# Kernel optimization log

Hardware: AMD Instinct MI355X
Metric: run time of the kernel (lower is better)

The kernel has to match this reference:

```python
import jax, jax.numpy as jnp
import numpy as np

H = 4  # num_heads

def _ln(x, g, b):
    m = x.mean(-1, keepdims=True)
    v = ((x - m) ** 2).mean(-1, keepdims=True)
    return (x - m) * jax.lax.rsqrt(v + 1e-5) * g + b

def _mlp(x, w1, b1, w2, b2):
    return jax.nn.relu(x @ w1 + b1) @ w2 + b2

def _lin_att(q, k, v):
    # q,k,v: [BB, L, H, hd] ; linear (kernelized) attention, no softmax
    L = q.shape[1]
    qn = q / jnp.maximum(jnp.linalg.norm(q, axis=-1, keepdims=True), 1e-12)
    kn = k / jnp.maximum(jnp.linalg.norm(k, axis=-1, keepdims=True), 1e-12)
    kvs = jnp.einsum('blhm,blhd->bhmd', kn, v)
    num = jnp.einsum('bnhm,bhmd->bnhd', qn, kvs) + L * v
    den = jnp.einsum('bnhm,bhm->bnh', qn, kn.sum(axis=1))[..., None] + L
    return num / den

def _fast_attn(x4, w_qkv, w_op, b_op):
    # x4: [B,T,N,D]; spatial attention over N, temporal attention over T, concat, project
    B, T, N, D = x4.shape
    hd = D // H
    q, k, v = jnp.split(x4 @ w_qkv, 3, axis=-1)
    sh = lambda t: t.reshape(B * T, N, H, hd)
    out_s = _lin_att(sh(q), sh(k), sh(v)).reshape(B, T, N, D)
    th = lambda t: jnp.swapaxes(t, 1, 2).reshape(B * N, T, H, hd)
    out_t = jnp.swapaxes(_lin_att(th(q), th(k), th(v)).reshape(B, N, T, D), 1, 2)
    return jnp.concatenate([out_s, out_t], axis=-1) @ w_op + b_op

def _forward(x, W_in, b_in, adp, W_tp, b_tp, qkv_w, op_w, op_b, pw_w, pw_b,
             fc_w1, fc_b1, fc_w2, fc_b2, ln1_g, ln1_b, ln2_g, ln2_b,
             ep_w, ep_b, enc_w1, enc_b1, enc_w2, enc_b2, out_w, out_b):
    Nn, T, _ = x.shape
    xt = jnp.swapaxes(x, 0, 1)[None]                 # [1,T,N,in]
    h = xt @ W_in + b_in                             # input_proj -> [1,T,N,24]
    h = jnp.concatenate([h, adp[None]], axis=-1)     # + adaptive emb -> [1,T,N,104]
    h = h @ W_tp + b_tp                              # temporal_proj: 1x1 conv == pointwise linear
    graph = jnp.einsum('tnd,tmd->tnm', adp, adp)     # [T,N,N]
    graph = jax.nn.softmax(jax.nn.relu(graph), axis=-1)  # AvgPool(1,1) is identity
    # GraphPropagate (order=2, eval/no-dropout): [h, graph @ h]
    z1 = jnp.einsum('tni,btid->btnd', graph, h)
    att0 = _fast_attn(h, qkv_w[0], op_w[0], op_b[0])
    att1 = _fast_attn(z1, qkv_w[1], op_w[1], op_b[1])
    # scale = [1, 0.01]; note torch's in-place aliasing makes ln1 input = 2*x_glo
    g = h + att0 * (h @ pw_w[0] + pw_b[0]) + 0.01 * att1 * (att0 @ pw_w[1] + pw_b[1])
    h1 = _ln(2.0 * g, ln1_g, ln1_b)
    h2 = _ln(h1 + _mlp(h1, fc_w1, fc_b1, fc_w2, fc_b2), ln2_g, ln2_b)
    y = jnp.swapaxes(h2, 1, 2).reshape(1, Nn, T * h2.shape[-1]) @ ep_w + ep_b  # encoder_proj
    for i in range(enc_w1.shape[0]):                 # 3 residual MLP blocks
        y = y + _mlp(y, enc_w1[i], enc_b1[i], enc_w2[i], enc_b2[i])
    out = y @ out_w + out_b                          # [1,N,365]
    return out.reshape(Nn, T, 1)

def setup_inputs() -> dict:
    key = jax.random.key(0)
    ks = jax.random.split(key, 24)
    f = lambda i, shape, s=0.05: jax.random.normal(ks[i], shape, dtype=jnp.float32) * s
    D, T, N, IN = 104, 365, 400, 3
    return {
        'x': jax.random.normal(ks[0], (N, T, IN), dtype=jnp.float32),
        'W_in': f(1, (IN, 24)), 'b_in': f(2, (24,)),
        'adp': f(3, (T, N, 80)),
        'W_tp': f(4, (D, D)), 'b_tp': f(5, (D,)),
        'qkv_w': f(6, (2, D, 3 * D)),
        'op_w': f(7, (2, 2 * D, D)), 'op_b': f(8, (2, D)),
        'pw_w': f(9, (2, D, D)), 'pw_b': f(10, (2, D)),
        'fc_w1': f(11, (D, 2 * D)), 'fc_b1': f(12, (2 * D,)),
        'fc_w2': f(13, (2 * D, D)), 'fc_b2': f(14, (D,)),
        'ln1_g': jnp.ones((D,), jnp.float32), 'ln1_b': jnp.zeros((D,), jnp.float32),
        'ln2_g': jnp.ones((D,), jnp.float32), 'ln2_b': jnp.zeros((D,), jnp.float32),
        'ep_w': f(15, (T * D, D), 0.01), 'ep_b': f(16, (D,)),
        'enc_w1': f(17, (3, D, 2 * D)), 'enc_b1': f(18, (3, 2 * D)),
        'enc_w2': f(19, (3, 2 * D, D)), 'enc_b2': f(20, (3, D)),
        'out_w': f(21, (D, T)), 'out_b': f(22, (T,)),
    }

def reference(x, W_in, b_in, adp, W_tp, b_tp, qkv_w, op_w, op_b, pw_w, pw_b,
              fc_w1, fc_b1, fc_w2, fc_b2, ln1_g, ln1_b, ln2_g, ln2_b,
              ep_w, ep_b, enc_w1, enc_b1, enc_w2, enc_b2, out_w, out_b):
    return _forward(x, W_in, b_in, adp, W_tp, b_tp, qkv_w, op_w, op_b, pw_w, pw_b,
                    fc_w1, fc_b1, fc_w2, fc_b2, ln1_g, ln1_b, ln2_g, ln2_b,
                    ep_w, ep_b, enc_w1, enc_b1, enc_w2, enc_b2, out_w, out_b)
```

## Files before the change

### kernel.cpp

```cpp
#include <hip/hip_runtime.h>
#include <hip/hip_bf16.h>
#include <cstddef>

#define TT   365
#define NN   400
#define TN   (TT*NN)
#define HD   26
#define NH   4

#define CEILDIV(a,b) (((a)+(b)-1)/(b))

typedef __hip_bfloat16 bf16;
typedef short short8v __attribute__((ext_vector_type(8)));
typedef float float4v __attribute__((ext_vector_type(4)));
typedef float float16v __attribute__((ext_vector_type(16)));
__device__ __forceinline__ float b2f(bf16 v){ return __bfloat162float(v); }
__device__ __forceinline__ bf16  f2b(float v){ return __float2bfloat16(v); }

static constexpr size_t NB0 = (size_t)TN*104;
static constexpr size_t NB1 = (size_t)TN*104;
static constexpr size_t NB2 = (size_t)TN*312;
static constexpr size_t NB3 = (size_t)TN*104;
static constexpr size_t NBF = NB0+NB1+NB2+NB3;
static constexpr size_t NTILE   = (size_t)108*32;
static constexpr size_t NKVSB_S = (size_t)TT*NTILE;
static constexpr size_t NKVSB_T = (size_t)NN*NTILE;
static constexpr size_t NY      = (size_t)NN*104;
static constexpr size_t NW_TP   = 104*128;
static constexpr size_t NW_QKV  = 312*128;
static constexpr size_t NW_OP   = 104*224;
static constexpr size_t NW_PW   = 104*128;
static constexpr size_t NW_FC1  = 208*128;
static constexpr size_t NW_FC2  = 104*224;
static constexpr size_t NW_EPT  = (size_t)104*37960;
static constexpr size_t NWT     = NW_TP + 2*NW_QKV + 2*NW_OP + 2*NW_PW + NW_FC1 + NW_FC2 + NW_EPT;
static constexpr size_t WS_NEEDED = NBF*2 + (NKVSB_S+NKVSB_T)*2 + NY*4 + NWT*2;
static constexpr size_t NADP_ROWS = (size_t)TN + 64;
static constexpr size_t NADP = NADP_ROWS*96;
static constexpr size_t NHT  = ((size_t)TT*104 + 8)*448;
static_assert(NADP + NHT <= NB2, "z1 scratch must fit in B2");

__global__ void __launch_bounds__(256) prep_w(
    const float* __restrict__ W, bf16* __restrict__ Wt, int K, int Nc, int KP)
{
    int idx = blockIdx.x*256 + threadIdx.x;
    if (idx >= Nc*KP) return;
    int n = idx / KP, k = idx - n*KP;
    Wt[idx] = (k < K) ? f2b(W[(size_t)k*Nc + n]) : f2b(0.f);
}

__global__ void __launch_bounds__(256) prep_wT(
    const float* __restrict__ W, bf16* __restrict__ Wt)
{
    __shared__ float T[64][105];
    int k0 = blockIdx.x * 64;
    int tid = threadIdx.x;
    for (int idx = tid; idx < 64*104; idx += 256) {
        int r = idx / 104, c = idx - r*104;
        int k = k0 + r;
        T[r][c] = (k < 37960) ? W[(size_t)k*104 + c] : 0.f;
    }
    __syncthreads();
    for (int idx = tid; idx < 104*32; idx += 256) {
        int n = idx >> 5, kp = idx & 31;
        int k = kp*2;
        if (k0 + k + 1 < 37960 || k0 + k < 37960) {
            if (k0 + k < 37960) {
                bf16 lo = f2b(T[k][n]);
                bf16 hi = f2b(T[k+1][n]);
                uint v = ((uint)(*(ushort*)&hi) << 16) | (*(ushort*)&lo);
                if (k0 + k + 1 < 37960) *(uint*)(Wt + (size_t)n*37960 + k0 + k) = v;
                else Wt[(size_t)n*37960 + k0 + k] = lo;
            }
        }
    }
}

__global__ void __launch_bounds__(256) prep_adp(
    const float* __restrict__ adp, bf16* __restrict__ out)
{
    size_t i = (size_t)blockIdx.x*256 + threadIdx.x;
    if (i >= NADP) return;
    size_t row = i / 96; int e = (int)(i - row*96);
    float v = (row < TN && e < 80) ? adp[row*80 + e] : 0.f;
    out[i] = f2b(v);
}

__global__ void __launch_bounds__(256) ht_kernel(
    const bf16* __restrict__ h, bf16* __restrict__ hT)
{
    __shared__ bf16 As[64*106];
    int t = blockIdx.y, n0 = blockIdx.x*64;
    int tid = threadIdx.x;
    for (int idx = tid; idx < 64*52; idx += 256) {
        int r = idx / 52, k = idx - r*52;
        int n = n0 + r;
        uint v = 0;
        if (n < NN) v = *(const uint*)(h + ((size_t)t*NN + n)*104 + k*2);
        *(uint*)(&As[r*106 + k*2]) = v;
    }
    __syncthreads();
    for (int idx = tid; idx < 104*32; idx += 256) {
        int d = idx >> 5, np = idx & 31;
        int n = np*2;
        ushort lo = *(ushort*)&As[n*106 + d];
        ushort hi = *(ushort*)&As[(n+1)*106 + d];
        uint v = ((uint)hi << 16) | lo;
        *(uint*)(hT + ((size_t)t*104 + d)*448 + n0 + n) = v;
    }
}

__global__ void __launch_bounds__(128) hcat_kernel(
    const float* __restrict__ x, const float* __restrict__ W_in,
    const float* __restrict__ b_in, const float* __restrict__ adp,
    bf16* __restrict__ hcat)
{
    int bid = blockIdx.x;
    int t = bid / NN, n = bid - t*NN;
    int tid = threadIdx.x;
    if (tid < 24) {
        float s = b_in[tid];
        size_t xb = ((size_t)n*TT + t)*3;
        #pragma unroll
        for (int i = 0; i < 3; ++i) s += x[xb + i] * W_in[i*24 + tid];
        hcat[(size_t)bid*104 + tid] = f2b(s);
    } else if (tid < 104) {
        hcat[(size_t)bid*104 + tid] = f2b(adp[(size_t)bid*80 + (tid - 24)]);
    }
}

template<int KP>
__global__ void __launch_bounds__(256) gemm_mf(
    const bf16* __restrict__ A, int lda, int K,
    const bf16* __restrict__ Wt, const float* __restrict__ bias,
    bf16* __restrict__ C, int M, int Nc, int relu)
{
    constexpr int STR = KP + 8;
    constexpr int KPQ = KP/8;
    __shared__ bf16 As[64*STR];
    __shared__ bf16 Ws[64*STR];
    int m0 = blockIdx.x * 64;
    int c0 = blockIdx.y * 64;
    int tid = threadIdx.x;
    const int KQ = K/8;
    uint4 z4 = {0u,0u,0u,0u};
    for (int idx = tid; idx < 64*KPQ; idx += 256) {
        int r = idx / KPQ, q = idx - r*KPQ;
        int m = m0 + r;
        uint4 v = z4;
        if (m < M && q < KQ) v = *(const uint4*)(A + (size_t)m*lda + q*8);
        *(uint4*)(&As[r*STR + q*8]) = v;
    }
    for (int idx = tid; idx < 64*KPQ; idx += 256) {
        int r = idx / KPQ, q = idx - r*KPQ;
        int n = c0 + r;
        uint4 v = z4;
        if (n < Nc) v = *(const uint4*)(Wt + (size_t)n*KP + q*8);
        *(uint4*)(&Ws[r*STR + q*8]) = v;
    }
    __syncthreads();

    int lane = tid & 63, w = tid >> 6;
    int n16 = lane & 15, quad = lane >> 4;
    constexpr int KS = KP/32;
    short8v af[KS];
    #pragma unroll
    for (int s = 0; s < KS; ++s)
        af[s] = *(const short8v*)(&As[(16*w + n16)*STR + s*32 + quad*8]);
    float4v acc[4];
    #pragma unroll
    for (int ct = 0; ct < 4; ++ct) { float4v z = {0.f,0.f,0.f,0.f}; acc[ct] = z; }
    #pragma unroll
    for (int ct = 0; ct < 4; ++ct) {
        #pragma unroll
        for (int s = 0; s < KS; ++s) {
            short8v bfr = *(const short8v*)(&Ws[(ct*16 + n16)*STR + s*32 + quad*8]);
            acc[ct] = __builtin_amdgcn_mfma_f32_16x16x32_bf16(af[s], bfr, acc[ct], 0, 0, 0);
        }
    }
    #pragma unroll
    for (int ct = 0; ct < 4; ++ct) {
        int c = c0 + ct*16 + n16;
        if (c < Nc) {
            float b = bias ? bias[c] : 0.f;
            #pragma unroll
            for (int reg = 0; reg < 4; ++reg) {
                int m = m0 + 16*w + quad*4 + reg;
                if (m < M) {
                    float v = acc[ct][reg] + b;
                    if (relu) v = fmaxf(v, 0.f);
                    C[(size_t)m*Nc + c] = f2b(v);
                }
            }
        }
    }
}

__global__ void __launch_bounds__(256) gate_ln1(
    bf16* __restrict__ h, const bf16* __restrict__ att0, const bf16* __restrict__ att1,
    const bf16* __restrict__ w0t, const bf16* __restrict__ w1t, const float* __restrict__ pwb,
    const float* __restrict__ gamma, const float* __restrict__ beta)
{
    constexpr int STR = 136;
    __shared__ bf16 A0s[64*STR];
    __shared__ bf16 A1s[64*STR];
    __shared__ bf16 Ws[112*STR];
    __shared__ float prm[416];
    int m0 = blockIdx.x * 64;
    int tid = threadIdx.x;
    int lane = tid & 63, w = tid >> 6, n16 = lane & 15, quad = lane >> 4;
    uint4 z4 = {0u,0u,0u,0u};

    for (int idx = tid; idx < 64*16; idx += 256) {
        int r = idx >> 4, q = idx & 15;
        int m = m0 + r;
        uint4 v0 = z4, v1 = z4;
        if (m < TN && q < 13) {
            v0 = *(const uint4*)(h    + (size_t)m*104 + q*8);
            v1 = *(const uint4*)(att0 + (size_t)m*104 + q*8);
        }
        *(uint4*)(&A0s[r*STR + q*8]) = v0;
        *(uint4*)(&A1s[r*STR + q*8]) = v1;
    }
    for (int idx = tid; idx < 112*16; idx += 256) {
        int c = idx >> 4, q = idx & 15;
        uint4 v = z4;
        if (c < 104) v = *(const uint4*)(w0t + (size_t)c*128 + q*8);
        *(uint4*)(&Ws[c*STR + q*8]) = v;
    }
    for (int i = tid; i < 416; i += 256)
        prm[i] = (i < 208) ? pwb[i] : (i < 312 ? gamma[i-208] : beta[i-312]);
    __syncthreads();

    short8v a0f[4], a1f[4];
    #pragma unroll
    for (int s = 0; s < 4; ++s) {
        a0f[s] = *(const short8v*)(&A0s[(16*w + n16)*STR + s*32 + quad*8]);
        a1f[s] = *(const short8v*)(&A1s[(16*w + n16)*STR + s*32 + quad*8]);
    }
    float4v acc0[7], acc1[7];
    #pragma unroll
    for (int ct = 0; ct < 7; ++ct) { float4v z = {0.f,0.f,0.f,0.f}; acc0[ct] = z; acc1[ct] = z; }
    #pragma unroll
    for (int ct = 0; ct < 7; ++ct)
        #pragma unroll
        for (int s = 0; s < 4; ++s) {
            short8v bfr = *(const short8v*)(&Ws[(ct*16 + n16)*STR + s*32 + quad*8]);
            acc0[ct] = __builtin_amdgcn_mfma_f32_16x16x32_bf16(a0f[s], bfr, acc0[ct], 0, 0, 0);
        }
    __syncthreads();
    for (int idx = tid; idx < 112*16; idx += 256) {
        int c = idx >> 4, q = idx & 15;
        uint4 v = z4;
        if (c < 104) v = *(const uint4*)(w1t + (size_t)c*128 + q*8);
        *(uint4*)(&Ws[c*STR + q*8]) = v;
    }
    __syncthreads();
    #pragma unroll
    for (int ct = 0; ct < 7; ++ct)
        #pragma unroll
        for (int s = 0; s < 4; ++s) {
            short8v bfr = *(const short8v*)(&Ws[(ct*16 + n16)*STR + s*32 + quad*8]);
            acc1[ct] = __builtin_amdgcn_mfma_f32_16x16x32_bf16(a1f[s], bfr, acc1[ct], 0, 0, 0);
        }

    float sum[4] = {0.f,0.f,0.f,0.f};
    #pragma unroll
    for (int ct = 0; ct < 7; ++ct) {
        int c = ct*16 + n16;
        bool colok = c < 104;
        float b0 = colok ? prm[c] : 0.f;
        float b1 = colok ? prm[104 + c] : 0.f;
        #pragma unroll
        for (int reg = 0; reg < 4; ++reg) {
            int r = 16*w + quad*4 + reg;
            int m = m0 + r;
            float xv = 0.f;
            if (colok && m < TN) {
                float p0 = acc0[ct][reg] + b0;
                float p1 = acc1[ct][reg] + b1;
                float hv = b2f(A0s[r*STR + c]);
                float a0 = b2f(A1s[r*STR + c]);
                float a1 = b2f(att1[(size_t)m*104 + c]);
                xv = 2.f*(hv + a0*p0 + 0.01f*a1*p1);
            }
            acc0[ct][reg] = xv;
            sum[reg] += xv;
        }
    }
    #pragma unroll
    for (int reg = 0; reg < 4; ++reg) {
        float v = sum[reg];
        v += __shfl_xor(v,1,64); v += __shfl_xor(v,2,64);
        v += __shfl_xor(v,4,64); v += __shfl_xor(v,8,64);
        sum[reg] = v * (1.f/104.f);
    }
    float var[4] = {0.f,0.f,0.f,0.f};
    #pragma unroll
    for (int ct = 0; ct < 7; ++ct) {
        bool colok = (ct*16 + n16) < 104;
        #pragma unroll
        for (int reg = 0; reg < 4; ++reg) {
            if (colok) {
                float d = acc0[ct][reg] - sum[reg];
                acc0[ct][reg] = d;
                var[reg] += d*d;
            }
        }
    }
    #pragma unroll
    for (int reg = 0; reg < 4; ++reg) {
        float v = var[reg];
        v += __shfl_xor(v,1,64); v += __shfl_xor(v,2,64);
        v += __shfl_xor(v,4,64); v += __shfl_xor(v,8,64);
        var[reg] = rsqrtf(v * (1.f/104.f) + 1e-5f);
    }
    #pragma unroll
    for (int ct = 0; ct < 7; ++ct) {
        int c = ct*16 + n16;
        if (c < 104) {
            float g = prm[208 + c], be = prm[312 + c];
            #pragma unroll
            for (int reg = 0; reg < 4; ++reg) {
                int m = m0 + 16*w + quad*4 + reg;
                if (m < TN)
                    h[(size_t)m*104 + c] = f2b(acc0[ct][reg]*var[reg]*g + be);
            }
        }
    }
}

__global__ void __launch_bounds__(256) fc2_ln2(
    const bf16* __restrict__ hidden, const bf16* __restrict__ w2t, const float* __restrict__ b2,
    const bf16* __restrict__ h1, const float* __restrict__ gamma, const float* __restrict__ beta,
    bf16* __restrict__ h2)
{
    constexpr int STRA = 232;
    constexpr int STRW = 136;
    __shared__ bf16 As[64*STRA];
    __shared__ bf16 Ws[112*STRW];
    __shared__ float prm[312];
    int m0 = blockIdx.x * 64;
    int tid = threadIdx.x;
    int lane = tid & 63, w = tid >> 6, n16 = lane & 15, quad = lane >> 4;
    uint4 z4 = {0u,0u,0u,0u};

    for (int idx = tid; idx < 64*28; idx += 256) {
        int r = idx / 28, q = idx - r*28;
        int m = m0 + r;
        uint4 v = z4;
        if (m < TN && q < 26) v = *(const uint4*)(hidden + (size_t)m*208 + q*8);
        *(uint4*)(&As[r*STRA + q*8]) = v;
    }
    for (int idx = tid; idx < 112*16; idx += 256) {
        int c = idx >> 4, q = idx & 15;
        uint4 v = z4;
        if (c < 104) v = *(const uint4*)(w2t + (size_t)c*224 + q*8);
        *(uint4*)(&Ws[c*STRW + q*8]) = v;
    }
    for (int i = tid; i < 312; i += 256)
        prm[i] = (i < 104) ? b2[i] : (i < 208 ? gamma[i-104] : beta[i-208]);
    __syncthreads();

    short8v af[7];
    #pragma unroll
    for (int s = 0; s < 7; ++s)
        af[s] = *(const short8v*)(&As[(16*w + n16)*STRA + s*32 + quad*8]);
    float4v acc[7];
    #pragma unroll
    for (int ct = 0; ct < 7; ++ct) { float4v z = {0.f,0.f,0.f,0.f}; acc[ct] = z; }
    #pragma unroll
    for (int ct = 0; ct < 7; ++ct)
        #pragma unroll
        for (int s = 0; s < 4; ++s) {
            short8v bfr = *(const short8v*)(&Ws[(ct*16 + n16)*STRW + s*32 + quad*8]);
            acc[ct] = __builtin_amdgcn_mfma_f32_16x16x32_bf16(af[s], bfr, acc[ct], 0, 0, 0);
        }
    __syncthreads();
    for (int idx = tid; idx < 112*16; idx += 256) {
        int c = idx >> 4, q = idx & 15;
        uint4 v = z4;
        if (c < 104 && q < 12) v = *(const uint4*)(w2t + (size_t)c*224 + 128 + q*8);
        *(uint4*)(&Ws[c*STRW + q*8]) = v;
    }
    __syncthreads();
    #pragma unroll
    for (int ct = 0; ct < 7; ++ct)
        #pragma unroll
        for (int s = 4; s < 7; ++s) {
            short8v bfr = *(const short8v*)(&Ws[(ct*16 + n16)*STRW + (s-4)*32 + quad*8]);
            acc[ct] = __builtin_amdgcn_mfma_f32_16x16x32_bf16(af[s], bfr, acc[ct], 0, 0, 0);
        }

    float sum[4] = {0.f,0.f,0.f,0.f};
    #pragma unroll
    for (int ct = 0; ct < 7; ++ct) {
        int c = ct*16 + n16;
        bool colok = c < 104;
        float bb = colok ? prm[c] : 0.f;
        #pragma unroll
        for (int reg = 0; reg < 4; ++reg) {
            int m = m0 + 16*w + quad*4 + reg;
            float xv = 0.f;
            if (colok && m < TN)
                xv = b2f(h1[(size_t)m*104 + c]) + acc[ct][reg] + bb;
            acc[ct][reg] = xv;
            sum[reg] += xv;
        }
    }
    #pragma unroll
    for (int reg = 0; reg < 4; ++reg) {
        float v = sum[reg];
        v += __shfl_xor(v,1,64); v += __shfl_xor(v,2,64);
        v += __shfl_xor(v,4,64); v += __shfl_xor(v,8,64);
        sum[reg] = v * (1.f/104.f);
    }
    float var[4] = {0.f,0.f,0.f,0.f};
    #pragma unroll
    for (int ct = 0; ct < 7; ++ct) {
        bool colok = (ct*16 + n16) < 104;
        #pragma unroll
        for (int reg = 0; reg < 4; ++reg) {
            if (colok) {
                float d = acc[ct][reg] - sum[reg];
                acc[ct][reg] = d;
                var[reg] += d*d;
            }
        }
    }
    #pragma unroll
    for (int reg = 0; reg < 4; ++reg) {
        float v = var[reg];
        v += __shfl_xor(v,1,64); v += __shfl_xor(v,2,64);
        v += __shfl_xor(v,4,64); v += __shfl_xor(v,8,64);
        var[reg] = rsqrtf(v * (1.f/104.f) + 1e-5f);
    }
    #pragma unroll
    for (int ct = 0; ct < 7; ++ct) {
        int c = ct*16 + n16;
        if (c < 104) {
            float g = prm[104 + c], be = prm[208 + c];
            #pragma unroll
            for (int reg = 0; reg < 4; ++reg) {
                int m = m0 + 16*w + quad*4 + reg;
                if (m < TN)
                    h2[(size_t)m*104 + c] = f2b(acc[ct][reg]*var[reg]*g + be);
            }
        }
    }
}

__global__ void __launch_bounds__(256) ep_mf(
    const bf16* __restrict__ h2, const bf16* __restrict__ wt, float* __restrict__ y)
{
    constexpr int STR = 136;
    __shared__ bf16 As[64*STR];
    __shared__ bf16 Ws[64*STR];
    int m0 = blockIdx.x * 64;
    int c0 = blockIdx.y * 64;
    int t0 = blockIdx.z * 8;
    int t1 = min(TT, t0 + 8);
    int tid = threadIdx.x;
    int lane = tid & 63, w = tid >> 6, n16 = lane & 15, quad = lane >> 4;
    uint4 z4 = {0u,0u,0u,0u};

    float4v acc[4];
    #pragma unroll
    for (int ct = 0; ct < 4; ++ct) { float4v z = {0.f,0.f,0.f,0.f}; acc[ct] = z; }

    for (int t = t0; t < t1; ++t) {
        for (int idx = tid; idx < 64*16; idx += 256) {
            int r = idx >> 4, q = idx & 15;
            int m = m0 + r;
            uint4 va = z4;
            if (m < NN && q < 13) va = *(const uint4*)(h2 + ((size_t)t*NN + m)*104 + q*8);
            *(uint4*)(&As[r*STR + q*8]) = va;
            int c = c0 + r;
            uint4 vw = z4;
            if (c < 104 && q < 13) vw = *(const uint4*)(wt + (size_t)c*37960 + t*104 + q*8);
            *(uint4*)(&Ws[r*STR + q*8]) = vw;
        }
        __syncthreads();
        short8v af[4];
        #pragma unroll
        for (int s = 0; s < 4; ++s)
            af[s] = *(const short8v*)(&As[(16*w + n16)*STR + s*32 + quad*8]);
        #pragma unroll
        for (int ct = 0; ct < 4; ++ct) {
            #pragma unroll
            for (int s = 0; s < 4; ++s) {
                short8v bfr = *(const short8v*)(&Ws[(ct*16 + n16)*STR + s*32 + quad*8]);
                acc[ct] = __builtin_amdgcn_mfma_f32_16x16x32_bf16(af[s], bfr, acc[ct], 0, 0, 0);
            }
        }
        __syncthreads();
    }
    #pragma unroll
    for (int ct = 0; ct < 4; ++ct) {
        int c = c0 + ct*16 + n16;
        if (c < 104) {
            #pragma unroll
            for (int reg = 0; reg < 4; ++reg) {
                int m = m0 + 16*w + quad*4 + reg;
                if (m < NN) atomicAdd(&y[(size_t)m*104 + c], acc[ct][reg]);
            }
        }
    }
}

__global__ void __launch_bounds__(256) z1_mf(
    const bf16* __restrict__ adp_bf, const bf16* __restrict__ hT, bf16* __restrict__ z1)
{
    constexpr int SA = 104;
    constexpr int SP = 72;
    __shared__ bf16 As[64*SA];
    __shared__ bf16 Bt[64*SA];
    __shared__ bf16 Ht[112*SP];
    __shared__ bf16 P[64*SP];
    int t = blockIdx.y;
    int r0 = blockIdx.x * 64;
    int tid = threadIdx.x;
    int lane = tid & 63, w = tid >> 6, n16 = lane & 15, quad = lane >> 4;

    {
        const uint4* src = (const uint4*)(adp_bf + ((size_t)t*NN + r0)*96);
        for (int idx = tid; idx < 768; idx += 256) {
            int r = idx / 12, q = idx - r*12;
            *(uint4*)(&As[r*SA + q*8]) = src[idx];
        }
    }
    __syncthreads();
    short8v af[3];
    #pragma unroll
    for (int s = 0; s < 3; ++s)
        af[s] = *(const short8v*)(&As[(16*w + n16)*SA + s*32 + quad*8]);

    float4v onum[7];
    #pragma unroll
    for (int dt = 0; dt < 7; ++dt) { float4v z = {0.f,0.f,0.f,0.f}; onum[dt] = z; }
    float rs[4] = {0.f,0.f,0.f,0.f};

    for (int c0 = 0; c0 < NN; c0 += 64) {
        {
            const uint4* srcB = (const uint4*)(adp_bf + ((size_t)t*NN + c0)*96);
            for (int idx = tid; idx < 768; idx += 256) {
                int r = idx / 12, q = idx - r*12;
                *(uint4*)(&Bt[r*SA + q*8]) = srcB[idx];
            }
        }
        {
            const bf16* hb = hT + (size_t)t*104*448 + c0;
            for (int idx = tid; idx < 896; idx += 256) {
                int d = idx >> 3, q = idx & 7;
                *(uint4*)(&Ht[d*SP + q*8]) = *(const uint4*)(hb + (size_t)d*448 + q*8);
            }
        }
        __syncthreads();
        float4v sc[4];
        #pragma unroll
        for (int ct = 0; ct < 4; ++ct) { float4v z = {0.f,0.f,0.f,0.f}; sc[ct] = z; }
        #pragma unroll
        for (int ct = 0; ct < 4; ++ct) {
            #pragma unroll
            for (int s = 0; s < 3; ++s) {
                short8v bfr = *(const short8v*)(&Bt[(ct*16 + n16)*SA + s*32 + quad*8]);
                sc[ct] = __builtin_amdgcn_mfma_f32_16x16x32_bf16(af[s], bfr, sc[ct], 0, 0, 0);
            }
        }
        #pragma unroll
        for (int ct = 0; ct < 4; ++ct) {
            bool colok = (c0 + ct*16 + n16) < NN;
            #pragma unroll
            for (int reg = 0; reg < 4; ++reg) {
                float e = colok ? __expf(fmaxf(sc[ct][reg], 0.f)) : 0.f;
                rs[reg] += e;
                P[(16*w + quad*4 + reg)*SP + ct*16 + n16] = f2b(e);
            }
        }
        short8v pf[2];
        #pragma unroll
        for (int s = 0; s < 2; ++s)
            pf[s] = *(const short8v*)(&P[(16*w + n16)*SP + s*32 + quad*8]);
        #pragma unroll
        for (int dt = 0; dt < 7; ++dt) {
            #pragma unroll
            for (int s = 0; s < 2; ++s) {
                short8v bfr = *(const short8v*)(&Ht[(dt*16 + n16)*SP + s*32 + quad*8]);
                onum[dt] = __builtin_amdgcn_mfma_f32_16x16x32_bf16(pf[s], bfr, onum[dt], 0, 0, 0);
            }
        }
        __syncthreads();
    }
    #pragma unroll
    for (int reg = 0; reg < 4; ++reg) {
        float v = rs[reg];
        v += __shfl_xor(v, 1, 64);
        v += __shfl_xor(v, 2, 64);
        v += __shfl_xor(v, 4, 64);
        v += __shfl_xor(v, 8, 64);
        rs[reg] = v;
    }
    #pragma unroll
    for (int reg = 0; reg < 4; ++reg) {
        int row = r0 + 16*w + quad*4 + reg;
        if (row < NN) {
            float inv = 1.f / rs[reg];
            #pragma unroll
            for (int dt = 0; dt < 7; ++dt) {
                int d = dt*16 + n16;
                if (d < 104)
                    z1[((size_t)t*NN + row)*104 + d] = f2b(onum[dt][reg] * inv);
            }
        }
    }
}

__global__ void __launch_bounds__(256) kvs_mf(
    const bf16* __restrict__ qkv, bf16* __restrict__ kvsb_s, bf16* __restrict__ kvsb_t)
{
    constexpr int CK = 32;
    constexpr int TS = 40;
    __shared__ bf16 raw[CK][216];
    __shared__ bf16 kTn[4][32][TS];
    __shared__ bf16 vT [4][32][TS];
    __shared__ float invs[CK][4];

    int bb = blockIdx.x;
    bf16* out; int L; long long strideL, base;
    if (bb < TT) { out = kvsb_s + (size_t)bb*NTILE; L = NN; base = (long long)bb*NN*312 + 104; strideL = 312; }
    else { int n = bb - TT; out = kvsb_t + (size_t)n*NTILE; L = TT; base = (long long)n*312 + 104; strideL = (long long)NN*312; }

    int tid = threadIdx.x;
    int lane = tid & 63, w = tid >> 6;
    int n32 = lane & 31, koct = lane >> 5;
    uint4 z4 = {0u,0u,0u,0u};

    float16v acc;
    #pragma unroll
    for (int i = 0; i < 16; ++i) acc[i] = 0.f;

    uint4 pre[4];
    #pragma unroll
    for (int j = 0; j < 4; ++j) {
        int idx = tid + j*256;
        uint4 v = z4;
        if (idx < CK*26) {
            int r = idx / 26, q = idx - r*26;
            if (r < L) v = *(const uint4*)(qkv + base + (long long)r*strideL + q*8);
        }
        pre[j] = v;
    }

    for (int l0 = 0; l0 < L; l0 += CK) {
        int lw = min(CK, L - l0);
        __syncthreads();
        #pragma unroll
        for (int j = 0; j < 4; ++j) {
            int idx = tid + j*256;
            if (idx < CK*26) {
                int r = idx / 26, q = idx - r*26;
                *(uint4*)(&raw[r][q*8]) = pre[j];
            }
        }
        __syncthreads();
        {
            int ln0 = l0 + CK;
            #pragma unroll
            for (int j = 0; j < 4; ++j) {
                int idx = tid + j*256;
                uint4 v = z4;
                if (idx < CK*26 && ln0 < L) {
                    int r = idx / 26, q = idx - r*26;
                    if (r < L - ln0) v = *(const uint4*)(qkv + base + (long long)(ln0 + r)*strideL + q*8);
                }
                pre[j] = v;
            }
        }
        if (tid < CK*4) {
            int l = tid >> 2, h = tid & 3;
            float ss = 0.f;
            #pragma unroll
            for (int m = 0; m < HD; ++m) { float v = b2f(raw[l][h*HD + m]); ss += v*v; }
            invs[l][h] = (l < lw) ? 1.f/fmaxf(sqrtf(ss), 1e-12f) : 0.f;
        }
        __syncthreads();
        for (int idx = tid; idx < 4*CK*HD; idx += 256) {
            int h = idx / (CK*HD); int rem = idx - h*CK*HD;
            int l = rem / HD; int m = rem - l*HD;
            float iv = invs[l][h];
            kTn[h][m][l] = f2b(b2f(raw[l][h*HD + m]) * iv);
            vT[h][m][l]  = raw[l][104 + h*HD + m];
        }
        if (tid < 4*CK) {
            int h = tid >> 5, l = tid & 31;
            vT[h][26][l] = f2b((l < lw) ? 1.f : 0.f);
        }
        __syncthreads();
        #pragma unroll
        for (int s = 0; s < 2; ++s) {
            short8v a = *(const short8v*)(&kTn[w][n32][s*16 + koct*8]);
            short8v b = *(const short8v*)(&vT [w][n32][s*16 + koct*8]);
            acc = __builtin_amdgcn_mfma_f32_32x32x16_bf16(a, b, acc, 0, 0, 0);
        }
    }

    int lo = w*HD;
    #pragma unroll
    for (int reg = 0; reg < 16; ++reg) {
        int m = (reg & 3) + 8*(reg >> 2) + 4*koct;
        if (m < HD) {
            if (n32 < HD)       out[(size_t)(lo + n32)*32 + m] = f2b(acc[reg]);
            else if (n32 == HD) out[(size_t)(104 + w)*32 + m] = f2b(acc[reg]);
        }
    }
}

__global__ void __launch_bounds__(256) attn_mm(
    bf16* __restrict__ qkv, const bf16* __restrict__ kvsb,
    int M, long long bStride, long long rowStride, float Lf, int outOff)
{
    constexpr int STR = 136;
    __shared__ bf16 As[64*STR];
    __shared__ bf16 Ws[112*STR];
    __shared__ float nsqL[64*4];
    __shared__ float denL[64*4];
    int mt = blockIdx.x, bb = blockIdx.y;
    int tid = threadIdx.x;
    int lane = tid & 63, w = tid >> 6, n16 = lane & 15, quad = lane >> 4;
    bf16* base = qkv + (size_t)bb * bStride;
    int r0 = mt*64;
    uint4 z4 = {0u,0u,0u,0u};

    for (int idx = tid; idx < 64*16; idx += 256) {
        int r = idx >> 4, q = idx & 15;
        int m = r0 + r;
        uint4 v = z4;
        if (m < M && q < 13) v = *(const uint4*)(base + (size_t)m*rowStride + q*8);
        *(uint4*)(&As[r*STR + q*8]) = v;
    }
    for (int idx = tid; idx < 112*16; idx += 256) {
        int c = idx >> 4, q = idx & 15;
        *(uint4*)(&Ws[c*STR + q*8]) = z4;
    }
    __syncthreads();
    {
        const bf16* kb = kvsb + (size_t)bb * NTILE;
        for (int idx = tid; idx < 108*13; idx += 256) {
            int c = idx / 13, qu = idx - c*13;
            int lo = (c < 104) ? (c/26)*26 : (c-104)*26;
            *(uint*)(&Ws[c*STR + lo + qu*2]) = *(const uint*)(kb + (size_t)c*32 + qu*2);
        }
    }
    __syncthreads();

    short8v af[4];
    #pragma unroll
    for (int s = 0; s < 4; ++s)
        af[s] = *(const short8v*)(&As[(16*w + n16)*STR + s*32 + quad*8]);
    float4v acc[7];
    #pragma unroll
    for (int ct = 0; ct < 7; ++ct) { float4v z = {0.f,0.f,0.f,0.f}; acc[ct] = z; }
    #pragma unroll
    for (int ct = 0; ct < 7; ++ct) {
        #pragma unroll
        for (int s = 0; s < 4; ++s) {
            short8v bfr = *(const short8v*)(&Ws[(ct*16 + n16)*STR + s*32 + quad*8]);
            acc[ct] = __builtin_amdgcn_mfma_f32_16x16x32_bf16(af[s], bfr, acc[ct], 0, 0, 0);
        }
    }
    {
        int row = tid >> 2, hh = tid & 3;
        const bf16* qr = &As[row*STR + hh*26];
        float ss = 0.f;
        #pragma unroll
        for (int m = 0; m < HD; ++m) { float v = b2f(qr[m]); ss += v*v; }
        nsqL[row*4 + hh] = ss;
    }
    if (n16 >= 8 && n16 < 12) {
        #pragma unroll
        for (int reg = 0; reg < 4; ++reg)
            denL[(16*w + quad*4 + reg)*4 + (n16 - 8)] = acc[6][reg];
    }
    __syncthreads();
    #pragma unroll
    for (int ct = 0; ct < 7; ++ct) {
        int c = ct*16 + n16;
        if (c < 104) {
            int hh = c / 26;
            #pragma unroll
            for (int reg = 0; reg < 4; ++reg) {
                int lr = 16*w + quad*4 + reg;
                int m = r0 + lr;
                if (m < M) {
                    float iq = 1.f / fmaxf(sqrtf(nsqL[lr*4 + hh]), 1e-12f);
                    float den = iq * denL[lr*4 + hh] + Lf;
                    bf16* rp = base + (size_t)m*rowStride;
                    float num = iq * acc[ct][reg] + Lf * b2f(rp[208 + c]);
                    rp[outOff + c] = f2b(num / den);
                }
            }
        }
    }
}

__global__ void __launch_bounds__(256) y_init_kernel(float* __restrict__ y, const float* __restrict__ ep_b) {
    int i = blockIdx.x*256 + threadIdx.x;
    if (i < NN*104) y[i] = ep_b[i % 104];
}

__global__ void __launch_bounds__(256) enc_kernel(
    float* __restrict__ y, const float* __restrict__ w1, const float* __restrict__ b1,
    const float* __restrict__ w2, const float* __restrict__ b2)
{
    int n = blockIdx.x;
    int tid = threadIdx.x;
    __shared__ float yr[104], hid[208];
    if (tid < 104) yr[tid] = y[(size_t)n*104 + tid];
    __syncthreads();
    if (tid < 208) {
        float s = b1[tid];
        for (int k = 0; k < 104; ++k) s += yr[k] * w1[(size_t)k*208 + tid];
        hid[tid] = fmaxf(s, 0.f);
    }
    __syncthreads();
    if (tid < 104) {
        float s = b2[tid];
        for (int k = 0; k < 208; ++k) s += hid[k] * w2[(size_t)k*104 + tid];
        y[(size_t)n*104 + tid] = yr[tid] + s;
    }
}

__global__ void __launch_bounds__(256) out_kernel(
    const float* __restrict__ y, const float* __restrict__ out_w,
    const float* __restrict__ out_b, float* __restrict__ out)
{
    int n = blockIdx.x;
    int tid = threadIdx.x;
    __shared__ float yr[104];
    if (tid < 104) yr[tid] = y[(size_t)n*104 + tid];
    __syncthreads();
    for (int t = tid; t < TT; t += 256) {
        float s = out_b[t];
        for (int d = 0; d < 104; ++d) s += yr[d] * out_w[(size_t)d*TT + t];
        out[(size_t)n*TT + t] = s;
    }
}

extern "C" void kernel_launch(void* const* d_in, const int* in_sizes, int n_in,
                              void* d_out, int out_size, void* d_ws, size_t ws_size,
                              hipStream_t stream) {
    if (ws_size < WS_NEEDED) return;

    const float* x      = (const float*)d_in[0];
    const float* W_in   = (const float*)d_in[1];
    const float* b_in   = (const float*)d_in[2];
    const float* adp    = (const float*)d_in[3];
    const float* W_tp   = (const float*)d_in[4];
    const float* b_tp   = (const float*)d_in[5];
    const float* qkv_w  = (const float*)d_in[6];
    const float* op_w   = (const float*)d_in[7];
    const float* op_b   = (const float*)d_in[8];
    const float* pw_w   = (const float*)d_in[9];
    const float* pw_b   = (const float*)d_in[10];
    const float* fc_w1  = (const float*)d_in[11];
    const float* fc_b1  = (const float*)d_in[12];
    const float* fc_w2  = (const float*)d_in[13];
    const float* fc_b2  = (const float*)d_in[14];
    const float* ln1_g  = (const float*)d_in[15];
    const float* ln1_b  = (const float*)d_in[16];
    const float* ln2_g  = (const float*)d_in[17];
    const float* ln2_b  = (const float*)d_in[18];
    const float* ep_w   = (const float*)d_in[19];
    const float* ep_b   = (const float*)d_in[20];
    const float* enc_w1 = (const float*)d_in[21];
    const float* enc_b1 = (const float*)d_in[22];
    const float* enc_w2 = (const float*)d_in[23];
    const float* enc_b2 = (const float*)d_in[24];
    const float* out_w  = (const float*)d_in[25];
    const float* out_b  = (const float*)d_in[26];

    bf16* B0 = (bf16*)d_ws;
    bf16* B1 = B0 + NB0;
    bf16* B2 = B1 + NB1;
    bf16* B3 = B2 + NB2;
    bf16* kvsb_s = B3 + NB3;
    bf16* kvsb_t = kvsb_s + NKVSB_S;
    float* ybuf  = (float*)(kvsb_t + NKVSB_T);
    bf16* wtp   = (bf16*)(ybuf + NY);
    bf16* wqkv0 = wtp + NW_TP;
    bf16* wqkv1 = wqkv0 + NW_QKV;
    bf16* wop0  = wqkv1 + NW_QKV;
    bf16* wop1  = wop0 + NW_OP;
    bf16* wpw0  = wop1 + NW_OP;
    bf16* wpw1  = wpw0 + NW_PW;
    bf16* wfc1  = wpw1 + NW_PW;
    bf16* wfc2  = wfc1 + NW_FC1;
    bf16* wept  = wfc2 + NW_FC2;
    bf16* adp_bf = B2;
    bf16* hTbuf  = B2 + NADP;

    prep_w<<<CEILDIV(104*128,256), 256, 0, stream>>>(W_tp, wtp, 104, 104, 128);
    prep_w<<<CEILDIV(312*128,256), 256, 0, stream>>>(qkv_w, wqkv0, 104, 312, 128);
    prep_w<<<CEILDIV(312*128,256), 256, 0, stream>>>(qkv_w + 104*312, wqkv1, 104, 312, 128);
    prep_w<<<CEILDIV(104*224,256), 256, 0, stream>>>(op_w, wop0, 208, 104, 224);
    prep_w<<<CEILDIV(104*224,256), 256, 0, stream>>>(op_w + 208*104, wop1, 208, 104, 224);
    prep_w<<<CEILDIV(104*128,256), 256, 0, stream>>>(pw_w, wpw0, 104, 104, 128);
    prep_w<<<CEILDIV(104*128,256), 256, 0, stream>>>(pw_w + 104*104, wpw1, 104, 104, 128);
    prep_w<<<CEILDIV(208*128,256), 256, 0, stream>>>(fc_w1, wfc1, 104, 208, 128);
    prep_w<<<CEILDIV(104*224,256), 256, 0, stream>>>(fc_w2, wfc2, 208, 104, 224);
    prep_wT<<<CEILDIV(37960,64), 256, 0, stream>>>(ep_w, wept);

    const int GX = CEILDIV(TN, 64);
    dim3 g4(GX, 4), g5(GX, 5);

    hcat_kernel<<<TN, 128, 0, stream>>>(x, W_in, b_in, adp, B2);
    gemm_mf<128><<<dim3(GX,2), 256, 0, stream>>>(B2, 104, 104, wtp, b_tp, B0, TN, 104, 0);
    prep_adp<<<CEILDIV((int)NADP,256), 256, 0, stream>>>(adp, adp_bf);
    ht_kernel<<<dim3(7, TT), 256, 0, stream>>>(B0, hTbuf);
    z1_mf<<<dim3(7, TT), 256, 0, stream>>>(adp_bf, hTbuf, B1);
    gemm_mf<128><<<g5, 256, 0, stream>>>(B0, 104, 104, wqkv0, nullptr, B2, TN, 312, 0);
    kvs_mf<<<TT+NN, 256, 0, stream>>>(B2, kvsb_s, kvsb_t);
    attn_mm<<<dim3(6, NN), 256, 0, stream>>>(B2, kvsb_t, TT, 312, (long long)NN*312, (float)TT, 104);
    attn_mm<<<dim3(7, TT), 256, 0, stream>>>(B2, kvsb_s, NN, (long long)NN*312, 312, (float)NN, 0);
    gemm_mf<224><<<dim3(GX,2), 256, 0, stream>>>(B2, 312, 208, wop0, op_b, B3, TN, 104, 0);
    gemm_mf<128><<<g5, 256, 0, stream>>>(B1, 104, 104, wqkv1, nullptr, B2, TN, 312, 0);
    kvs_mf<<<TT+NN, 256, 0, stream>>>(B2, kvsb_s, kvsb_t);
    attn_mm<<<dim3(6, NN), 256, 0, stream>>>(B2, kvsb_t, TT, 312, (long long)NN*312, (float)TT, 104);
    attn_mm<<<dim3(7, TT), 256, 0, stream>>>(B2, kvsb_s, NN, (long long)NN*312, 312, (float)NN, 0);
    gemm_mf<224><<<dim3(GX,2), 256, 0, stream>>>(B2, 312, 208, wop1, op_b + 104, B1, TN, 104, 0);
    gate_ln1<<<GX, 256, 0, stream>>>(B0, B3, B1, wpw0, wpw1, pw_b, ln1_g, ln1_b);
    gemm_mf<128><<<g4, 256, 0, stream>>>(B0, 104, 104, wfc1, fc_b1, B2, TN, 208, 1);
    fc2_ln2<<<GX, 256, 0, stream>>>(B2, wfc2, fc_b2, B0, ln2_g, ln2_b, B3);
    y_init_kernel<<<CEILDIV(NN*104,256), 256, 0, stream>>>(ybuf, ep_b);
    ep_mf<<<dim3(CEILDIV(NN,64), 2, CEILDIV(TT,8)), 256, 0, stream>>>(B3, wept, ybuf);
    for (int i = 0; i < 3; ++i)
        enc_kernel<<<NN, 256, 0, stream>>>(ybuf, enc_w1 + (size_t)i*104*208, enc_b1 + (size_t)i*208,
                                           enc_w2 + (size_t)i*208*104, enc_b2 + (size_t)i*104);
    out_kernel<<<NN, 256, 0, stream>>>(ybuf, out_w, out_b, (float*)d_out);
}
```

Measured before the change: 1.350 ms.

## Prefetch z1 tiles into registers, alias LDS, remap blocks per XCD

The z1 kernel now loads the next adp and hT tiles into registers while the current tile is being computed, which overlaps global loads with MFMA work. It also shrinks shared memory by aliasing the A buffer onto the H buffer and trimming H to 104 rows, and sets launch bounds to allow 4 blocks per CU. Blocks are remapped so that all row blocks of a given time step land on the same XCD, improving L2 reuse of that step's adp and hT. In exchange it needs more registers for the prefetch buffers and an extra barrier.

```diff
diff --git a/kernel.cpp b/kernel.cpp
--- a/kernel.cpp
+++ b/kernel.cpp
@@ -508,17 +508,26 @@
     }
 }
 
-__global__ void __launch_bounds__(256) z1_mf(
+static constexpr int Z1_TQ = CEILDIV(TT, 8);
+static constexpr int Z1_BLOCKS = 8 * Z1_TQ * 7;
+__global__ void __launch_bounds__(256, 4) z1_mf(
     const bf16* __restrict__ adp_bf, const bf16* __restrict__ hT, bf16* __restrict__ z1)
 {
     constexpr int SA = 104;
     constexpr int SP = 72;
-    __shared__ bf16 As[64*SA];
     __shared__ bf16 Bt[64*SA];
-    __shared__ bf16 Ht[112*SP];
+    __shared__ bf16 Hs[104*SP];
     __shared__ bf16 P[64*SP];
-    int t = blockIdx.y;
-    int r0 = blockIdx.x * 64;
+    bf16* As = Hs;
+
+    int bid = blockIdx.x;
+    int xcd = bid & 7;
+    int j = bid >> 3;
+    int tq = j / 7, rblk = j - tq*7;
+    int t = tq*8 + xcd;
+    if (t >= TT) return;
+    int r0 = rblk*64;
+
     int tid = threadIdx.x;
     int lane = tid & 63, w = tid >> 6, n16 = lane & 15, quad = lane >> 4;
 
@@ -534,28 +543,62 @@
     #pragma unroll
     for (int s = 0; s < 3; ++s)
         af[s] = *(const short8v*)(&As[(16*w + n16)*SA + s*32 + quad*8]);
+    __syncthreads();
 
     float4v onum[7];
     #pragma unroll
     for (int dt = 0; dt < 7; ++dt) { float4v z = {0.f,0.f,0.f,0.f}; onum[dt] = z; }
     float rs[4] = {0.f,0.f,0.f,0.f};
 
+    uint4 preB[3], preH[4];
+    {
+        const uint4* srcB = (const uint4*)(adp_bf + (size_t)t*NN*96);
+        #pragma unroll
+        for (int j2 = 0; j2 < 3; ++j2) preB[j2] = srcB[tid + j2*256];
+        const bf16* hb = hT + (size_t)t*104*448;
+        #pragma unroll
+        for (int j2 = 0; j2 < 4; ++j2) {
+            int idx = tid + j2*256;
+            uint4 v = {0u,0u,0u,0u};
+            if (idx < 832) {
+                int d = idx >> 3, q = idx & 7;
+                v = *(const uint4*)(hb + (size_t)d*448 + q*8);
+            }
+            preH[j2] = v;
+        }
+    }
+
     for (int c0 = 0; c0 < NN; c0 += 64) {
-        {
-            const uint4* srcB = (const uint4*)(adp_bf + ((size_t)t*NN + c0)*96);
-            for (int idx = tid; idx < 768; idx += 256) {
-                int r = idx / 12, q = idx - r*12;
-                *(uint4*)(&Bt[r*SA + q*8]) = srcB[idx];
-            }
-        }
-        {
-            const bf16* hb = hT + (size_t)t*104*448 + c0;
-            for (int idx = tid; idx < 896; idx += 256) {
+        #pragma unroll
+        for (int j2 = 0; j2 < 3; ++j2) {
+            int idx = tid + j2*256;
+            int r = idx / 12, q = idx - r*12;
+            *(uint4*)(&Bt[r*SA + q*8]) = preB[j2];
+        }
+        #pragma unroll
+        for (int j2 = 0; j2 < 4; ++j2) {
+            int idx = tid + j2*256;
+            if (idx < 832) {
                 int d = idx >> 3, q = idx & 7;
-                *(uint4*)(&Ht[d*SP + q*8]) = *(const uint4*)(hb + (size_t)d*448 + q*8);
+                *(uint4*)(&Hs[d*SP + q*8]) = preH[j2];
             }
         }
         __syncthreads();
+        int cn = c0 + 64;
+        if (cn < NN) {
+            const uint4* srcB = (const uint4*)(adp_bf + ((size_t)t*NN + cn)*96);
+            #pragma unroll
+            for (int j2 = 0; j2 < 3; ++j2) preB[j2] = srcB[tid + j2*256];
+            const bf16* hb = hT + (size_t)t*104*448 + cn;
+            #pragma unroll
+            for (int j2 = 0; j2 < 4; ++j2) {
+                int idx = tid + j2*256;
+                if (idx < 832) {
+                    int d = idx >> 3, q = idx & 7;
+                    preH[j2] = *(const uint4*)(hb + (size_t)d*448 + q*8);
+                }
+            }
+        }
         float4v sc[4];
         #pragma unroll
         for (int ct = 0; ct < 4; ++ct) { float4v z = {0.f,0.f,0.f,0.f}; sc[ct] = z; }
@@ -583,9 +626,11 @@
             pf[s] = *(const short8v*)(&P[(16*w + n16)*SP + s*32 + quad*8]);
         #pragma unroll
         for (int dt = 0; dt < 7; ++dt) {
+            int hr = dt*16 + n16;
+            if (hr > 103) hr = 103;
             #pragma unroll
             for (int s = 0; s < 2; ++s) {
-                short8v bfr = *(const short8v*)(&Ht[(dt*16 + n16)*SP + s*32 + quad*8]);
+                short8v bfr = *(const short8v*)(&Hs[hr*SP + s*32 + quad*8]);
                 onum[dt] = __builtin_amdgcn_mfma_f32_16x16x32_bf16(pf[s], bfr, onum[dt], 0, 0, 0);
             }
         }
@@ -917,7 +962,7 @@
     gemm_mf<128><<<dim3(GX,2), 256, 0, stream>>>(B2, 104, 104, wtp, b_tp, B0, TN, 104, 0);
     prep_adp<<<CEILDIV((int)NADP,256), 256, 0, stream>>>(adp, adp_bf);
     ht_kernel<<<dim3(7, TT), 256, 0, stream>>>(B0, hTbuf);
-    z1_mf<<<dim3(7, TT), 256, 0, stream>>>(adp_bf, hTbuf, B1);
+    z1_mf<<<Z1_BLOCKS, 256, 0, stream>>>(adp_bf, hTbuf, B1);
     gemm_mf<128><<<g5, 256, 0, stream>>>(B0, 104, 104, wqkv0, nullptr, B2, TN, 312, 0);
     kvs_mf<<<TT+NN, 256, 0, stream>>>(B2, kvsb_s, kvsb_t);
     attn_mm<<<dim3(6, NN), 256, 0, stream>>>(B2, kvsb_t, TT, 312, (long long)NN*312, (float)TT, 104);
```

After: 1.339 ms. No clear change (-0.9%).
